# Kernel tuning notes

Measured on AMD Instinct MI355X. Metric: run time of the kernel, lower is better.

The kernel has to match this reference:

```python
import jax, jax.numpy as jnp
import numpy as np

PATCH_SIDE = 20  # hardcoded in GenericCamera.project


def _resize_ac(img, out_h, out_w):
    """Bilinear resize with align_corners=True, matching F.interpolate. img: (B,C,H,W)."""
    B, C, H, W = img.shape
    ys = jnp.arange(out_h, dtype=jnp.float32) * (np.float32(H - 1) / np.float32(out_h - 1))
    xs = jnp.arange(out_w, dtype=jnp.float32) * (np.float32(W - 1) / np.float32(out_w - 1))
    y0 = jnp.floor(ys).astype(jnp.int32); y1 = jnp.minimum(y0 + 1, H - 1)
    x0 = jnp.floor(xs).astype(jnp.int32); x1 = jnp.minimum(x0 + 1, W - 1)
    wy = (ys - y0.astype(jnp.float32)).astype(img.dtype)
    wx = (xs - x0.astype(jnp.float32)).astype(img.dtype)
    top = img[:, :, y0, :] * (1 - wy)[None, None, :, None] + img[:, :, y1, :] * wy[None, None, :, None]
    return top[:, :, :, x0] * (1 - wx) + top[:, :, :, x1] * wx


def setup_inputs() -> dict:
    key = jax.random.key(0)
    k1, k2 = jax.random.split(key)
    B, H, W = 1, 128, 416
    R = jax.random.normal(k1, (B, 3, H, W), dtype=jnp.float32)
    X = jax.random.normal(k2, (B, 3, H, W), dtype=jnp.float32)
    return {"R": R, "X": X, "progress": 10}


def reference(R, X, progress):
    B, C, H_full, W_full = X.shape
    kh = PATCH_SIDE
    Ks = 2 * kh + 1          # 41
    K = Ks * Ks              # 1681
    H, W = H_full // 2, W_full // 2  # downsample=True

    ray = _resize_ac(R, H, W)          # (1,3,H,W)
    direction = _resize_ac(X, H, W)    # (1,3,H,W)

    # clamped patch window start per row/col (boundary shift logic of _get_patch_coords)
    sx = jnp.clip(jnp.arange(H) - kh, 0, H - 1 - 2 * kh)   # (H,)
    sy = jnp.clip(jnp.arange(W) - kh, 0, W - 1 - 2 * kh)   # (W,)
    off = jnp.arange(Ks)
    cx = sx[:, None] + off[None, :]    # (H,41) row indices of patch
    cy = sy[:, None] + off[None, :]    # (W,41) col indices of patch

    # separable patch gather: (3,H,W) -> (3,H,41,W) -> (3,H,41,W,41)
    r = ray[0]
    patch = r[:, cx, :][:, :, :, cy]                       # (3,H,41,W,41)
    patch = patch.transpose(0, 1, 3, 2, 4).reshape(3, H * W, K)  # (3,N,K)

    dirn = direction.reshape(B, 3, H * W)
    dirn = dirn / jnp.linalg.norm(dirn, axis=1, keepdims=True)
    d = dirn[0]                                            # (3,N)

    logits = jnp.einsum('cn,cnk->nk', d, patch)            # (N,K)
    temperature = np.float32(max(1e-8, 1e-4 / np.exp(0.1 * float(progress))))
    sm = jax.nn.softmax(logits / temperature, axis=-1)     # (N,K)

    # soft-argmax over patch coordinates (coords stored as (x,y) = (row,col))
    px = jnp.broadcast_to(cx[:, None, :, None], (H, W, Ks, Ks)).reshape(H * W, K).astype(jnp.float32)
    py = jnp.broadcast_to(cy[None, :, None, :], (H, W, Ks, Ks)).reshape(H * W, K).astype(jnp.float32)
    ix = jnp.einsum('nk,nk->n', sm, px).reshape(H, W)
    iy = jnp.einsum('nk,nk->n', sm, py).reshape(H, W)

    Xn = 2.0 * ix / (H - 1) - 1.0
    Yn = 2.0 * iy / (W - 1) - 1.0
    Xn = _resize_ac(Xn[None, None], H_full, W_full)[0, 0]
    Yn = _resize_ac(Yn[None, None], H_full, W_full)[0, 0]
    return jnp.stack([Yn, Xn], axis=-1).reshape(B, H_full, W_full, 2)
```

## Files before the change

### kernel.cpp

```cpp
#include <hip/hip_runtime.h>
#include <math.h>

#define HS 64
#define WS 208
#define HF 128
#define WF 416
#define NS (HS * WS)
#define KH 20
#define KS 41
#define KK (KS * KS)
#define NJ 27

__device__ __forceinline__ void ac_idx(int o, int inN, float sc, int& i0, int& i1, float& w) {
#pragma clang fp contract(off)
    float s = (float)o * sc;
    float f = floorf(s);
    i0 = (int)f;
    i1 = min(i0 + 1, inN - 1);
    w = s - f;
}

__global__ void k_down(const float* __restrict__ R, const float* __restrict__ X,
                       const int* __restrict__ prog,
                       float4* __restrict__ ray4, float4* __restrict__ dir4,
                       float* __restrict__ tbuf) {
#pragma clang fp contract(off)
    int n = blockIdx.x * blockDim.x + threadIdx.x;
    if (n >= NS) return;
    if (n == 0) {
        double T64 = fmax(1e-8, 1e-4 / exp(0.1 * (double)prog[0]));
        tbuf[0] = (float)T64;
    }
    int y = n / WS, x = n - y * WS;
    int y0, y1, x0, x1; float wy, wx;
    ac_idx(y, HF, 127.0f / 63.0f, y0, y1, wy);
    ac_idx(x, WF, 415.0f / 207.0f, x0, x1, wx);
    float omwy = 1.0f - wy, omwx = 1.0f - wx;
    float r[3], d[3];
#pragma unroll
    for (int c = 0; c < 3; ++c) {
        const float* p = R + c * (HF * WF);
        float v00 = p[y0 * WF + x0], v10 = p[y1 * WF + x0];
        float v01 = p[y0 * WF + x1], v11 = p[y1 * WF + x1];
        float a0 = v00 * omwy; float b0 = v10 * wy; float t0 = a0 + b0;
        float a1 = v01 * omwy; float b1 = v11 * wy; float t1 = a1 + b1;
        float c0 = t0 * omwx; float c1 = t1 * wx;
        r[c] = c0 + c1;
        const float* q = X + c * (HF * WF);
        float u00 = q[y0 * WF + x0], u10 = q[y1 * WF + x0];
        float u01 = q[y0 * WF + x1], u11 = q[y1 * WF + x1];
        float e0 = u00 * omwy; float f0 = u10 * wy; float s0 = e0 + f0;
        float e1 = u01 * omwy; float f1 = u11 * wy; float s1 = e1 + f1;
        float g0 = s0 * omwx; float g1 = s1 * wx;
        d[c] = g0 + g1;
    }
    float q0 = d[0] * d[0]; float q1 = d[1] * d[1]; float q2 = d[2] * d[2];
    float ssq = (q0 + q1) + q2;
    float nrm = (float)sqrt((double)ssq);
    ray4[n] = make_float4(r[0], r[1], r[2], 0.0f);
    dir4[n] = make_float4(d[0] / nrm, d[1] / nrm, d[2] / nrm, 0.0f);
}

__global__ __launch_bounds__(256) void k_main(const float4* __restrict__ ray4,
                                              const float4* __restrict__ dir4,
                                              const float* __restrict__ tbuf,
                                              float* __restrict__ xn, float* __restrict__ yn) {
#pragma clang fp contract(off)
    int wid = (int)((blockIdx.x * blockDim.x + threadIdx.x) >> 6);
    int lane = (int)(threadIdx.x & 63);
    if (wid >= NS) return;
    int h = wid / WS, w = wid - h * WS;
    int srow = min(max(h - KH, 0), HS - 1 - 2 * KH);
    int scol = min(max(w - KH, 0), WS - 1 - 2 * KH);

    float4 dv = dir4[wid];
    float d0 = dv.x, d1 = dv.y, d2 = dv.z;
    float Tf = tbuf[0];

    int k1i = (lane >= KS) ? 1 : 0;
    int k2i = lane - k1i * KS;
    int off = srow * WS + scol + k1i * WS + k2i;
    int colk = k2i;

    float lg[NJ]; float m = -INFINITY;
#pragma unroll
    for (int j = 0; j < NJ - 1; ++j) {
        float4 v = ray4[off];
        float p0 = d0 * v.x; float p1 = d1 * v.y; float p2 = d2 * v.z;
        float l = (p0 + p1) + p2;
        lg[j] = l;
        m = fmaxf(m, l);
        int cn = colk + 23;
        bool cr = cn >= KS;
        colk = cr ? cn - KS : cn;
        off += cr ? (2 * WS - 18) : (WS + 23);
    }
    {
        float l = -INFINITY;
        if (lane < KK - 64 * (NJ - 1)) {
            float4 v = ray4[off];
            float p0 = d0 * v.x; float p1 = d1 * v.y; float p2 = d2 * v.z;
            l = (p0 + p1) + p2;
        }
        lg[NJ - 1] = l;
        m = fmaxf(m, l);
    }
#pragma unroll
    for (int s = 1; s < 64; s <<= 1) m = fmaxf(m, __shfl_xor(m, s));

    float zm = m / Tf;
    float thresh = m - 0.004f;

    float se = 0.f, sr = 0.f, sc = 0.f;
#pragma unroll
    for (int j = 0; j < NJ; ++j) {
        if (__ballot(lg[j] > thresh)) {
            bool a = lg[j] > thresh;
            int k = lane + 64 * j;
            int kk1 = k / KS;
            int kk2 = k - kk1 * KS;
            float z = lg[j] / Tf;
            float arg = (z - zm) * 1.442695040888963f;
            float e = a ? __builtin_amdgcn_exp2f(arg) : 0.0f;
            se += e;
            sr += e * (float)(srow + kk1);
            sc += e * (float)(scol + kk2);
        }
    }
#pragma unroll
    for (int s = 1; s < 64; s <<= 1) {
        se += __shfl_xor(se, s);
        sr += __shfl_xor(sr, s);
        sc += __shfl_xor(sc, s);
    }
    if (lane == 0) {
        double ix = (double)sr / (double)se, iy = (double)sc / (double)se;
        xn[wid] = (float)(2.0 * ix / (double)(HS - 1) - 1.0);
        yn[wid] = (float)(2.0 * iy / (double)(WS - 1) - 1.0);
    }
}

__global__ void k_up(const float* __restrict__ xn, const float* __restrict__ yn,
                     float* __restrict__ out) {
#pragma clang fp contract(off)
    int i = blockIdx.x * blockDim.x + threadIdx.x;
    if (i >= HF * WF) return;
    int hh = i / WF, ww = i - hh * WF;
    int y0, y1, x0, x1; float wy, wx;
    ac_idx(hh, HS, 63.0f / 127.0f, y0, y1, wy);
    ac_idx(ww, WS, 207.0f / 415.0f, x0, x1, wx);
    float omwy = 1.0f - wy, omwx = 1.0f - wx;
    float a0, b0, t0, t1;
    a0 = xn[y0 * WS + x0] * omwy; b0 = xn[y1 * WS + x0] * wy; t0 = a0 + b0;
    a0 = xn[y0 * WS + x1] * omwy; b0 = xn[y1 * WS + x1] * wy; t1 = a0 + b0;
    float bx = t0 * omwx + t1 * wx;
    a0 = yn[y0 * WS + x0] * omwy; b0 = yn[y1 * WS + x0] * wy; t0 = a0 + b0;
    a0 = yn[y0 * WS + x1] * omwy; b0 = yn[y1 * WS + x1] * wy; t1 = a0 + b0;
    float ay = t0 * omwx + t1 * wx;
    out[2 * i]     = ay;
    out[2 * i + 1] = bx;
}

extern "C" void kernel_launch(void* const* d_in, const int* in_sizes, int n_in,
                              void* d_out, int out_size, void* d_ws, size_t ws_size,
                              hipStream_t stream) {
    const float* R = (const float*)d_in[0];
    const float* X = (const float*)d_in[1];
    const int* prog = (const int*)d_in[2];
    float4* ray4 = (float4*)d_ws;
    float4* dir4 = ray4 + NS;
    float* xn   = (float*)(dir4 + NS);
    float* yn   = xn + NS;
    float* tbuf = yn + NS;
    float* out  = (float*)d_out;

    k_down<<<(NS + 255) / 256, 256, 0, stream>>>(R, X, prog, ray4, dir4, tbuf);
    k_main<<<(NS * 64 + 255) / 256, 256, 0, stream>>>(ray4, dir4, tbuf, xn, yn);
    k_up<<<(HF * WF + 255) / 256, 256, 0, stream>>>(xn, yn, out);
}
```

Baseline: 31.38 us.

## Process two adjacent output pixels per wavefront in main softmax kernel

Each wavefront now handles two horizontally adjacent pixels, sharing index computation, the row offset walk, and the reduction loop structure, and loading the two patch windows at an offset of delta. This halves the wave count and amortizes per-wave overhead such as address math, shuffles and ballots across two pixels. In exchange it doubles register use for the logit arrays, which may reduce occupancy, and the two loads per step hit largely overlapping cache lines.

```diff
diff --git a/kernel.cpp b/kernel.cpp
--- a/kernel.cpp
+++ b/kernel.cpp
@@ -66,77 +66,102 @@
                                               const float* __restrict__ tbuf,
                                               float* __restrict__ xn, float* __restrict__ yn) {
 #pragma clang fp contract(off)
-    int wid = (int)((blockIdx.x * blockDim.x + threadIdx.x) >> 6);
+    int wave = (int)((blockIdx.x * blockDim.x + threadIdx.x) >> 6);
     int lane = (int)(threadIdx.x & 63);
-    if (wid >= NS) return;
-    int h = wid / WS, w = wid - h * WS;
+    int wa = wave * 2;
+    if (wa >= NS) return;
+    int h = wa / WS, w = wa - h * WS;
     int srow = min(max(h - KH, 0), HS - 1 - 2 * KH);
-    int scol = min(max(w - KH, 0), WS - 1 - 2 * KH);
-
-    float4 dv = dir4[wid];
-    float d0 = dv.x, d1 = dv.y, d2 = dv.z;
+    int sca  = min(max(w - KH, 0), WS - 1 - 2 * KH);
+    int scb  = min(max(w + 1 - KH, 0), WS - 1 - 2 * KH);
+    int delta = scb - sca;
+
+    float4 da4 = dir4[wa];
+    float4 db4 = dir4[wa + 1];
+    float a0c = da4.x, a1c = da4.y, a2c = da4.z;
+    float b0c = db4.x, b1c = db4.y, b2c = db4.z;
     float Tf = tbuf[0];
 
     int k1i = (lane >= KS) ? 1 : 0;
     int k2i = lane - k1i * KS;
-    int off = srow * WS + scol + k1i * WS + k2i;
+    int off = (srow + k1i) * WS + sca + k2i;
     int colk = k2i;
 
-    float lg[NJ]; float m = -INFINITY;
+    float lga[NJ], lgb[NJ];
+    float ma = -INFINITY, mb = -INFINITY;
 #pragma unroll
     for (int j = 0; j < NJ - 1; ++j) {
-        float4 v = ray4[off];
-        float p0 = d0 * v.x; float p1 = d1 * v.y; float p2 = d2 * v.z;
-        float l = (p0 + p1) + p2;
-        lg[j] = l;
-        m = fmaxf(m, l);
+        float4 va = ray4[off];
+        float4 vb = ray4[off + delta];
+        float pa0 = a0c * va.x; float pa1 = a1c * va.y; float pa2 = a2c * va.z;
+        float la = (pa0 + pa1) + pa2;
+        float pb0 = b0c * vb.x; float pb1 = b1c * vb.y; float pb2 = b2c * vb.z;
+        float lb = (pb0 + pb1) + pb2;
+        lga[j] = la; lgb[j] = lb;
+        ma = fmaxf(ma, la); mb = fmaxf(mb, lb);
         int cn = colk + 23;
         bool cr = cn >= KS;
         colk = cr ? cn - KS : cn;
         off += cr ? (2 * WS - 18) : (WS + 23);
     }
     {
-        float l = -INFINITY;
+        float la = -INFINITY, lb = -INFINITY;
         if (lane < KK - 64 * (NJ - 1)) {
-            float4 v = ray4[off];
-            float p0 = d0 * v.x; float p1 = d1 * v.y; float p2 = d2 * v.z;
-            l = (p0 + p1) + p2;
+            float4 va = ray4[off];
+            float4 vb = ray4[off + delta];
+            float pa0 = a0c * va.x; float pa1 = a1c * va.y; float pa2 = a2c * va.z;
+            la = (pa0 + pa1) + pa2;
+            float pb0 = b0c * vb.x; float pb1 = b1c * vb.y; float pb2 = b2c * vb.z;
+            lb = (pb0 + pb1) + pb2;
         }
-        lg[NJ - 1] = l;
-        m = fmaxf(m, l);
-    }
-#pragma unroll
-    for (int s = 1; s < 64; s <<= 1) m = fmaxf(m, __shfl_xor(m, s));
-
-    float zm = m / Tf;
-    float thresh = m - 0.004f;
-
-    float se = 0.f, sr = 0.f, sc = 0.f;
+        lga[NJ - 1] = la; lgb[NJ - 1] = lb;
+        ma = fmaxf(ma, la); mb = fmaxf(mb, lb);
+    }
+#pragma unroll
+    for (int s = 1; s < 64; s <<= 1) {
+        ma = fmaxf(ma, __shfl_xor(ma, s));
+        mb = fmaxf(mb, __shfl_xor(mb, s));
+    }
+
+    float zma = ma / Tf, zmb = mb / Tf;
+    float tha = ma - 0.004f, thb = mb - 0.004f;
+
+    float sea = 0.f, sra = 0.f, sca_ = 0.f;
+    float seb = 0.f, srb = 0.f, scb_ = 0.f;
 #pragma unroll
     for (int j = 0; j < NJ; ++j) {
-        if (__ballot(lg[j] > thresh)) {
-            bool a = lg[j] > thresh;
+        bool la = lga[j] > tha, lb = lgb[j] > thb;
+        if (__ballot(la || lb)) {
             int k = lane + 64 * j;
             int kk1 = k / KS;
             int kk2 = k - kk1 * KS;
-            float z = lg[j] / Tf;
-            float arg = (z - zm) * 1.442695040888963f;
-            float e = a ? __builtin_amdgcn_exp2f(arg) : 0.0f;
-            se += e;
-            sr += e * (float)(srow + kk1);
-            sc += e * (float)(scol + kk2);
+            float fr = (float)(srow + kk1);
+            if (__ballot(la)) {
+                float z = lga[j] / Tf;
+                float arg = (z - zma) * 1.442695040888963f;
+                float e = la ? __builtin_amdgcn_exp2f(arg) : 0.0f;
+                sea += e; sra += e * fr; sca_ += e * (float)(sca + kk2);
+            }
+            if (__ballot(lb)) {
+                float z = lgb[j] / Tf;
+                float arg = (z - zmb) * 1.442695040888963f;
+                float e = lb ? __builtin_amdgcn_exp2f(arg) : 0.0f;
+                seb += e; srb += e * fr; scb_ += e * (float)(scb + kk2);
+            }
         }
     }
 #pragma unroll
     for (int s = 1; s < 64; s <<= 1) {
-        se += __shfl_xor(se, s);
-        sr += __shfl_xor(sr, s);
-        sc += __shfl_xor(sc, s);
+        sea += __shfl_xor(sea, s); sra += __shfl_xor(sra, s); sca_ += __shfl_xor(sca_, s);
+        seb += __shfl_xor(seb, s); srb += __shfl_xor(srb, s); scb_ += __shfl_xor(scb_, s);
     }
     if (lane == 0) {
-        double ix = (double)sr / (double)se, iy = (double)sc / (double)se;
-        xn[wid] = (float)(2.0 * ix / (double)(HS - 1) - 1.0);
-        yn[wid] = (float)(2.0 * iy / (double)(WS - 1) - 1.0);
+        double ixa = (double)sra / (double)sea, iya = (double)sca_ / (double)sea;
+        xn[wa] = (float)(2.0 * ixa / (double)(HS - 1) - 1.0);
+        yn[wa] = (float)(2.0 * iya / (double)(WS - 1) - 1.0);
+        double ixb = (double)srb / (double)seb, iyb = (double)scb_ / (double)seb;
+        xn[wa + 1] = (float)(2.0 * ixb / (double)(HS - 1) - 1.0);
+        yn[wa + 1] = (float)(2.0 * iyb / (double)(WS - 1) - 1.0);
     }
 }
 
@@ -175,6 +200,6 @@
     float* out  = (float*)d_out;
 
     k_down<<<(NS + 255) / 256, 256, 0, stream>>>(R, X, prog, ray4, dir4, tbuf);
-    k_main<<<(NS * 64 + 255) / 256, 256, 0, stream>>>(ray4, dir4, tbuf, xn, yn);
+    k_main<<<(NS * 32 + 255) / 256, 256, 0, stream>>>(ray4, dir4, tbuf, xn, yn);
     k_up<<<(HF * WF + 255) / 256, 256, 0, stream>>>(xn, yn, out);
 }
```

Result: slower. 34.03 us (+8.5%).

## Assign one 256-thread block per pixel instead of one wavefront

Applied to the files above, without the earlier changes.

The main softmax kernel now gives each output pixel a whole 256-thread block (four wavefronts) rather than a single 64-lane wavefront. Each thread handles 7 patch elements instead of 27, and the max and the three partial sums are combined across wavefronts through shared memory with two block barriers. The aim is to cut per-thread serial work and register use so that more independent loads are in flight. The cost is four times as many threads, extra synchronisation, and a larger grid of small blocks.

```diff
diff --git a/kernel.cpp b/kernel.cpp
--- a/kernel.cpp
+++ b/kernel.cpp
@@ -9,7 +9,7 @@
 #define KH 20
 #define KS 41
 #define KK (KS * KS)
-#define NJ 27
+#define NJ2 7
 
 __device__ __forceinline__ void ac_idx(int o, int inN, float sc, int& i0, int& i1, float& w) {
 #pragma clang fp contract(off)
@@ -66,66 +66,76 @@
                                               const float* __restrict__ tbuf,
                                               float* __restrict__ xn, float* __restrict__ yn) {
 #pragma clang fp contract(off)
-    int wid = (int)((blockIdx.x * blockDim.x + threadIdx.x) >> 6);
-    int lane = (int)(threadIdx.x & 63);
-    if (wid >= NS) return;
-    int h = wid / WS, w = wid - h * WS;
+    int pix = blockIdx.x;
+    int tid = (int)threadIdx.x;
+    int lane = tid & 63;
+    int wid = tid >> 6;
+    int h = pix / WS, w = pix - h * WS;
     int srow = min(max(h - KH, 0), HS - 1 - 2 * KH);
     int scol = min(max(w - KH, 0), WS - 1 - 2 * KH);
 
-    float4 dv = dir4[wid];
+    float4 dv = dir4[pix];
     float d0 = dv.x, d1 = dv.y, d2 = dv.z;
     float Tf = tbuf[0];
 
-    int k1i = (lane >= KS) ? 1 : 0;
-    int k2i = lane - k1i * KS;
-    int off = srow * WS + scol + k1i * WS + k2i;
+    int k1i = (tid * 25) >> 10;
+    int k2i = tid - k1i * KS;
+    int off = (srow + k1i) * WS + scol + k2i;
     int colk = k2i;
 
-    float lg[NJ]; float m = -INFINITY;
+    float lg[NJ2];
+    float m = -INFINITY;
 #pragma unroll
-    for (int j = 0; j < NJ - 1; ++j) {
+    for (int j = 0; j < NJ2 - 1; ++j) {
         float4 v = ray4[off];
         float p0 = d0 * v.x; float p1 = d1 * v.y; float p2 = d2 * v.z;
         float l = (p0 + p1) + p2;
         lg[j] = l;
         m = fmaxf(m, l);
-        int cn = colk + 23;
+        int cn = colk + 10;
         bool cr = cn >= KS;
         colk = cr ? cn - KS : cn;
-        off += cr ? (2 * WS - 18) : (WS + 23);
+        off += cr ? (7 * WS - 31) : (6 * WS + 10);
     }
     {
         float l = -INFINITY;
-        if (lane < KK - 64 * (NJ - 1)) {
+        if (tid < KK - 256 * (NJ2 - 1)) {
             float4 v = ray4[off];
             float p0 = d0 * v.x; float p1 = d1 * v.y; float p2 = d2 * v.z;
             l = (p0 + p1) + p2;
         }
-        lg[NJ - 1] = l;
+        lg[NJ2 - 1] = l;
         m = fmaxf(m, l);
     }
 #pragma unroll
     for (int s = 1; s < 64; s <<= 1) m = fmaxf(m, __shfl_xor(m, s));
 
+    __shared__ float smax[4];
+    __shared__ float ssum[4][3];
+    if (lane == 0) smax[wid] = m;
+    __syncthreads();
+    m = fmaxf(fmaxf(smax[0], smax[1]), fmaxf(smax[2], smax[3]));
+
     float zm = m / Tf;
     float thresh = m - 0.004f;
 
     float se = 0.f, sr = 0.f, sc = 0.f;
+    int c1 = k1i, c2 = k2i;
 #pragma unroll
-    for (int j = 0; j < NJ; ++j) {
-        if (__ballot(lg[j] > thresh)) {
-            bool a = lg[j] > thresh;
-            int k = lane + 64 * j;
-            int kk1 = k / KS;
-            int kk2 = k - kk1 * KS;
+    for (int j = 0; j < NJ2; ++j) {
+        bool a = lg[j] > thresh;
+        if (__ballot(a)) {
             float z = lg[j] / Tf;
             float arg = (z - zm) * 1.442695040888963f;
             float e = a ? __builtin_amdgcn_exp2f(arg) : 0.0f;
             se += e;
-            sr += e * (float)(srow + kk1);
-            sc += e * (float)(scol + kk2);
+            sr += e * (float)(srow + c1);
+            sc += e * (float)(scol + c2);
         }
+        int cn = c2 + 10;
+        bool cr = cn >= KS;
+        c2 = cr ? cn - KS : cn;
+        c1 += cr ? 7 : 6;
     }
 #pragma unroll
     for (int s = 1; s < 64; s <<= 1) {
@@ -133,10 +143,15 @@
         sr += __shfl_xor(sr, s);
         sc += __shfl_xor(sc, s);
     }
-    if (lane == 0) {
-        double ix = (double)sr / (double)se, iy = (double)sc / (double)se;
-        xn[wid] = (float)(2.0 * ix / (double)(HS - 1) - 1.0);
-        yn[wid] = (float)(2.0 * iy / (double)(WS - 1) - 1.0);
+    if (lane == 0) { ssum[wid][0] = se; ssum[wid][1] = sr; ssum[wid][2] = sc; }
+    __syncthreads();
+    if (tid == 0) {
+        float SE = (ssum[0][0] + ssum[1][0]) + (ssum[2][0] + ssum[3][0]);
+        float SR = (ssum[0][1] + ssum[1][1]) + (ssum[2][1] + ssum[3][1]);
+        float SC = (ssum[0][2] + ssum[1][2]) + (ssum[2][2] + ssum[3][2]);
+        double ix = (double)SR / (double)SE, iy = (double)SC / (double)SE;
+        xn[pix] = (float)(2.0 * ix / (double)(HS - 1) - 1.0);
+        yn[pix] = (float)(2.0 * iy / (double)(WS - 1) - 1.0);
     }
 }
 
@@ -175,6 +190,6 @@
     float* out  = (float*)d_out;
 
     k_down<<<(NS + 255) / 256, 256, 0, stream>>>(R, X, prog, ray4, dir4, tbuf);
-    k_main<<<(NS * 64 + 255) / 256, 256, 0, stream>>>(ray4, dir4, tbuf, xn, yn);
+    k_main<<<NS, 256, 0, stream>>>(ray4, dir4, tbuf, xn, yn);
     k_up<<<(HF * WF + 255) / 256, 256, 0, stream>>>(xn, yn, out);
 }
```

New measurement: 30.79 us. No clear change (-1.9%).

## Process eight adjacent pixels per wave sharing one union patch load

Applied to the files above, without the earlier changes.

Each wave now handles 8 horizontally adjacent pixels. It loads the 41x48 union of their patches once and computes dot products for all 8 directions per loaded ray vector, which cuts redundant global/L2 traffic by roughly 8x. Candidate positions near each running max are recorded in per-pixel bitmasks. A second pass then re-reads only those positions to accumulate exponentials, replacing the full second sweep over the logits. The cost is more registers per thread (8 sets of accumulators) and fewer waves launched, which reduces parallelism; the mask heuristic also depends on the 0.005 margin being safe.

```diff
diff --git a/kernel.cpp b/kernel.cpp
--- a/kernel.cpp
+++ b/kernel.cpp
@@ -9,7 +9,11 @@
 #define KH 20
 #define KS 41
 #define KK (KS * KS)
-#define NJ 27
+#define UCOL 48
+#define GEL (KS * UCOL)
+#define NIT 31
+#define NWAVE (64 * 26)
+#define LOG2E 1.442695040888963f
 
 __device__ __forceinline__ void ac_idx(int o, int inN, float sc, int& i0, int& i1, float& w) {
 #pragma clang fp contract(off)
@@ -61,82 +65,107 @@
     dir4[n] = make_float4(d[0] / nrm, d[1] / nrm, d[2] / nrm, 0.0f);
 }
 
-__global__ __launch_bounds__(256) void k_main(const float4* __restrict__ ray4,
+__global__ __launch_bounds__(128) void k_main(const float4* __restrict__ ray4,
                                               const float4* __restrict__ dir4,
                                               const float* __restrict__ tbuf,
                                               float* __restrict__ xn, float* __restrict__ yn) {
 #pragma clang fp contract(off)
-    int wid = (int)((blockIdx.x * blockDim.x + threadIdx.x) >> 6);
-    int lane = (int)(threadIdx.x & 63);
-    if (wid >= NS) return;
-    int h = wid / WS, w = wid - h * WS;
-    int srow = min(max(h - KH, 0), HS - 1 - 2 * KH);
-    int scol = min(max(w - KH, 0), WS - 1 - 2 * KH);
-
-    float4 dv = dir4[wid];
-    float d0 = dv.x, d1 = dv.y, d2 = dv.z;
+    int tid = (int)threadIdx.x;
+    int lane = tid & 63;
+    int gw = (int)blockIdx.x * 2 + (tid >> 6);
+    int row = (gw * 2521) >> 16;
+    int grp = gw - row * 26;
+    int w0 = grp * 8;
+    int srow = min(max(row - KH, 0), HS - 1 - 2 * KH);
+    int scol0 = min(max(w0 - KH, 0), WS - 1 - 2 * KH);
     float Tf = tbuf[0];
 
-    int k1i = (lane >= KS) ? 1 : 0;
-    int k2i = lane - k1i * KS;
-    int off = srow * WS + scol + k1i * WS + k2i;
-    int colk = k2i;
-
-    float lg[NJ]; float m = -INFINITY;
-#pragma unroll
-    for (int j = 0; j < NJ - 1; ++j) {
-        float4 v = ray4[off];
-        float p0 = d0 * v.x; float p1 = d1 * v.y; float p2 = d2 * v.z;
-        float l = (p0 + p1) + p2;
-        lg[j] = l;
-        m = fmaxf(m, l);
-        int cn = colk + 23;
-        bool cr = cn >= KS;
-        colk = cr ? cn - KS : cn;
-        off += cr ? (2 * WS - 18) : (WS + 23);
-    }
-    {
-        float l = -INFINITY;
-        if (lane < KK - 64 * (NJ - 1)) {
-            float4 v = ray4[off];
-            float p0 = d0 * v.x; float p1 = d1 * v.y; float p2 = d2 * v.z;
-            l = (p0 + p1) + p2;
-        }
-        lg[NJ - 1] = l;
-        m = fmaxf(m, l);
-    }
-#pragma unroll
-    for (int s = 1; s < 64; s <<= 1) m = fmaxf(m, __shfl_xor(m, s));
-
-    float zm = m / Tf;
-    float thresh = m - 0.004f;
-
-    float se = 0.f, sr = 0.f, sc = 0.f;
-#pragma unroll
-    for (int j = 0; j < NJ; ++j) {
-        if (__ballot(lg[j] > thresh)) {
-            bool a = lg[j] > thresh;
-            int k = lane + 64 * j;
-            int kk1 = k / KS;
-            int kk2 = k - kk1 * KS;
-            float z = lg[j] / Tf;
-            float arg = (z - zm) * 1.442695040888963f;
-            float e = a ? __builtin_amdgcn_exp2f(arg) : 0.0f;
-            se += e;
-            sr += e * (float)(srow + kk1);
-            sc += e * (float)(scol + kk2);
+    float d0[8], d1[8], d2[8];
+    int dJ[8];
+#pragma unroll
+    for (int i = 0; i < 8; ++i) {
+        float4 dv = dir4[row * WS + w0 + i];
+        d0[i] = dv.x; d1[i] = dv.y; d2[i] = dv.z;
+        dJ[i] = min(max(w0 + i - KH, 0), WS - 1 - 2 * KH) - scol0;
+    }
+    int base = srow * WS + scol0;
+
+    float m[8];
+    unsigned msk[8];
+#pragma unroll
+    for (int i = 0; i < 8; ++i) { m[i] = -INFINITY; msk[i] = 0u; }
+#pragma unroll
+    for (int it = 0; it < NIT; ++it) {
+        if (it < NIT - 1 || lane < GEL - 64 * (NIT - 1)) {
+            int e = lane + 64 * it;
+            int rho = (e * 683) >> 15;
+            int j = e - rho * UCOL;
+            float4 v = ray4[base + rho * WS + j];
+#pragma unroll
+            for (int i = 0; i < 8; ++i) {
+                float p0 = d0[i] * v.x; float p1 = d1[i] * v.y; float p2 = d2[i] * v.z;
+                float l = (p0 + p1) + p2;
+                int c = j - dJ[i];
+                bool valid = (unsigned)c <= 40u;
+                float lv = valid ? l : -INFINITY;
+                bool f = (lv + 0.005f) > m[i];
+                msk[i] |= f ? (1u << it) : 0u;
+                m[i] = fmaxf(m[i], lv);
+            }
         }
     }
 #pragma unroll
     for (int s = 1; s < 64; s <<= 1) {
-        se += __shfl_xor(se, s);
-        sr += __shfl_xor(sr, s);
-        sc += __shfl_xor(sc, s);
+#pragma unroll
+        for (int i = 0; i < 8; ++i) m[i] = fmaxf(m[i], __shfl_xor(m[i], s));
+    }
+
+    float se[8], sr[8], sc[8];
+#pragma unroll
+    for (int i = 0; i < 8; ++i) { se[i] = 0.f; sr[i] = 0.f; sc[i] = 0.f; }
+#pragma unroll
+    for (int i = 0; i < 8; ++i) {
+        unsigned w8 = msk[i];
+        if (__ballot(w8 != 0u)) {
+            float th = m[i] - 0.004f;
+            float zm = m[i] / Tf;
+            while (w8) {
+                int it = __ffs(w8) - 1;
+                w8 &= w8 - 1;
+                int e = lane + (it << 6);
+                int rho = (e * 683) >> 15;
+                int j = e - rho * UCOL;
+                float4 v = ray4[base + rho * WS + j];
+                float p0 = d0[i] * v.x; float p1 = d1[i] * v.y; float p2 = d2[i] * v.z;
+                float l = (p0 + p1) + p2;
+                if (l > th) {
+                    float z = l / Tf;
+                    float e2 = __builtin_amdgcn_exp2f((z - zm) * LOG2E);
+                    se[i] += e2;
+                    sr[i] += e2 * (float)(srow + rho);
+                    sc[i] += e2 * (float)(scol0 + j);
+                }
+            }
+        }
+    }
+#pragma unroll
+    for (int s = 1; s < 64; s <<= 1) {
+#pragma unroll
+        for (int i = 0; i < 8; ++i) {
+            se[i] += __shfl_xor(se[i], s);
+            sr[i] += __shfl_xor(sr[i], s);
+            sc[i] += __shfl_xor(sc[i], s);
+        }
     }
     if (lane == 0) {
-        double ix = (double)sr / (double)se, iy = (double)sc / (double)se;
-        xn[wid] = (float)(2.0 * ix / (double)(HS - 1) - 1.0);
-        yn[wid] = (float)(2.0 * iy / (double)(WS - 1) - 1.0);
+#pragma unroll
+        for (int i = 0; i < 8; ++i) {
+            int pix = row * WS + w0 + i;
+            double ix = (double)sr[i] / (double)se[i];
+            double iy = (double)sc[i] / (double)se[i];
+            xn[pix] = (float)(2.0 * ix / (double)(HS - 1) - 1.0);
+            yn[pix] = (float)(2.0 * iy / (double)(WS - 1) - 1.0);
+        }
     }
 }
 
@@ -175,6 +204,6 @@
     float* out  = (float*)d_out;
 
     k_down<<<(NS + 255) / 256, 256, 0, stream>>>(R, X, prog, ray4, dir4, tbuf);
-    k_main<<<(NS * 64 + 255) / 256, 256, 0, stream>>>(ray4, dir4, tbuf, xn, yn);
+    k_main<<<NWAVE / 2, 128, 0, stream>>>(ray4, dir4, tbuf, xn, yn);
     k_up<<<(HF * WF + 255) / 256, 256, 0, stream>>>(xn, yn, out);
 }
```

Result: slower. 62.35 us (+98.7%).
